# Kernel tuning notes

Measured on AMD Instinct MI355X. Metric: run time of the kernel, lower is better.

Reference implementation:

```python
import jax, jax.numpy as jnp
import numpy as np

B, S, D = 4, 512, 256
NEG = -1e30  # finite stand-in for -inf so fully-masked row 0 stays NaN-free


def setup_inputs() -> dict:
    key = jax.random.key(0)
    ks = jax.random.split(key, 10)
    s = 0.02
    return {
        "x": jax.random.normal(ks[0], (B, S, D), dtype=jnp.float32),
        # edge_mlp: Linear(3D -> D), ReLU, Linear(D -> 1). Stored [in, out].
        "W1": jax.random.normal(ks[1], (3 * D, D), dtype=jnp.float32) * s,
        "b1": jnp.zeros((D,), dtype=jnp.float32),
        "w2": jax.random.normal(ks[2], (D, 1), dtype=jnp.float32) * s,
        "b2": jnp.zeros((1,), dtype=jnp.float32),
        "Wv": jax.random.normal(ks[3], (D, D), dtype=jnp.float32) * s,
        "bv": jnp.zeros((D,), dtype=jnp.float32),
        "Wo": jax.random.normal(ks[4], (D, D), dtype=jnp.float32) * s,
        "bo": jnp.zeros((D,), dtype=jnp.float32),
        "gamma": jnp.ones((D,), dtype=jnp.float32),
        "beta": jnp.zeros((D,), dtype=jnp.float32),
    }


def reference(x, W1, b1, w2, b2, Wv, bv, Wo, bo, gamma, beta):
    b, seq, d = x.shape
    # edge_mlp layer1 on concat([x_i, x_j, x_i - x_j]) decomposes linearly:
    # h[b,i,j,:] = x_i @ (Wa + Wc) + x_j @ (Wb - Wc) + b1
    Wa, Wb, Wc = W1[:d], W1[d:2 * d], W1[2 * d:]
    hi = jnp.einsum('bid,dh->bih', x, Wa + Wc)          # [B,S,D]
    hj = jnp.einsum('bjd,dh->bjh', x, Wb - Wc)          # [B,S,D]
    h = jax.nn.relu(hi[:, :, None, :] + hj[:, None, :, :] + b1)  # [B,S,S,D]
    scores = jnp.einsum('bijh,h->bij', h, w2[:, 0]) + b2[0]      # [B,S,S]
    # strictly-lower-triangular causal mask (j < i)
    mask = jnp.tril(jnp.ones((seq, seq), dtype=bool), k=-1)
    scores = jnp.where(mask, scores, NEG)
    attn = jax.nn.softmax(scores, axis=-1)
    # row i=0 has no valid edges (torch yields NaN there); zero it instead
    row_valid = mask.any(axis=-1)                       # [S]
    attn = attn * row_valid[None, :, None].astype(attn.dtype)
    values = jnp.einsum('bjd,de->bje', x, Wv) + bv      # [B,S,D]
    message = jnp.einsum('bij,bjd->bid', attn, values)  # [B,S,D]
    out = jnp.einsum('bid,de->bie', message, Wo) + bo
    out = x + out
    # LayerNorm over last dim, eps=1e-5, biased variance (torch default)
    mu = jnp.mean(out, axis=-1, keepdims=True)
    var = jnp.mean(jnp.square(out - mu), axis=-1, keepdims=True)
    out = (out - mu) * jax.lax.rsqrt(var + 1e-5) * gamma + beta
    return out
```

## Files before the change

kernel.cpp:

```cpp
#include <hip/hip_runtime.h>
#include <math.h>

#define D 256
#define S 512
#define M 2048

typedef __attribute__((ext_vector_type(8))) short bf16x8;
typedef __attribute__((ext_vector_type(4))) float f32x4;

__device__ inline ushort f2bf(float f) {
    union { float f; unsigned u; } v; v.f = f;
    unsigned r = v.u + 0x7FFFu + ((v.u >> 16) & 1u);
    return (ushort)(r >> 16);
}

__global__ __launch_bounds__(256) void pack_w(
    const float* __restrict__ W1, const float* __restrict__ Wv,
    const float* __restrict__ Wo, ushort* __restrict__ WAt,
    ushort* __restrict__ WBt, ushort* __restrict__ Wvt, ushort* __restrict__ Wot)
{
    const int blk = blockIdx.x, t = threadIdx.x;
    const int mat = blk >> 4;
    const int a0 = ((blk >> 2) & 3) * 64;
    const int b0 = (blk & 3) * 64;
    __shared__ ushort lt[64][72];
    const int r = t >> 4;
    const int c = (t & 15) * 4;
#pragma unroll
    for (int p = 0; p < 4; ++p) {
        const int sr = b0 + p * 16 + r;
        float4 v;
        if (mat == 0) {
            float4 wa = *(const float4*)(W1 + (size_t)sr * 256 + a0 + c);
            float4 wc = *(const float4*)(W1 + (size_t)(512 + sr) * 256 + a0 + c);
            v = make_float4(wa.x + wc.x, wa.y + wc.y, wa.z + wc.z, wa.w + wc.w);
        } else if (mat == 1) {
            float4 wb = *(const float4*)(W1 + (size_t)(256 + sr) * 256 + a0 + c);
            float4 wc = *(const float4*)(W1 + (size_t)(512 + sr) * 256 + a0 + c);
            v = make_float4(wb.x - wc.x, wb.y - wc.y, wb.z - wc.z, wb.w - wc.w);
        } else if (mat == 2) {
            v = *(const float4*)(Wv + (size_t)sr * 256 + a0 + c);
        } else {
            v = *(const float4*)(Wo + (size_t)sr * 256 + a0 + c);
        }
        lt[p * 16 + r][c + 0] = f2bf(v.x);
        lt[p * 16 + r][c + 1] = f2bf(v.y);
        lt[p * 16 + r][c + 2] = f2bf(v.z);
        lt[p * 16 + r][c + 3] = f2bf(v.w);
    }
    __syncthreads();
    ushort* dst = (mat == 0) ? WAt : (mat == 1) ? WBt : (mat == 2) ? Wvt : Wot;
#pragma unroll
    for (int p = 0; p < 4; ++p) {
        const int dr = p * 16 + r;
        ushort4 o = make_ushort4(lt[c + 0][dr], lt[c + 1][dr],
                                 lt[c + 2][dr], lt[c + 3][dr]);
        *(ushort4*)(dst + (size_t)(a0 + dr) * 256 + b0 + c) = o;
    }
}

__global__ __launch_bounds__(256) void gemm_qkv_mfma(
    const float* __restrict__ x, const ushort* __restrict__ WAt,
    const ushort* __restrict__ WBt, const ushort* __restrict__ Wvt,
    const float* __restrict__ b1, const float* __restrict__ bv,
    float* __restrict__ hi, float* __restrict__ hj, ushort* __restrict__ vals_t)
{
    const int bn = blockIdx.x, bm = blockIdx.y;
    const int n0 = bn * 64, m0 = bm * 64;
    const int region = n0 >> 8, c0 = n0 & 255;
    const ushort* Bt = (region == 0) ? WAt : (region == 1) ? WBt : Wvt;
    const int t = threadIdx.x, w = t >> 6, l = t & 63;
    const int q = l >> 4, ln = l & 15;
    const int wm = (w >> 1) * 32, wn = (w & 1) * 32;

    __shared__ ushort T[64][72];

    f32x4 acc[2][2] = {};
    for (int k0 = 0; k0 < 256; k0 += 32) {
        union { bf16x8 v; ushort s[8]; } a[2];
        bf16x8 b[2];
#pragma unroll
        for (int mt = 0; mt < 2; ++mt) {
            const float* xr = x + (size_t)(m0 + wm + mt * 16 + ln) * 256 + k0 + q * 8;
            float4 u0 = *(const float4*)xr;
            float4 u1 = *(const float4*)(xr + 4);
            a[mt].s[0] = f2bf(u0.x); a[mt].s[1] = f2bf(u0.y);
            a[mt].s[2] = f2bf(u0.z); a[mt].s[3] = f2bf(u0.w);
            a[mt].s[4] = f2bf(u1.x); a[mt].s[5] = f2bf(u1.y);
            a[mt].s[6] = f2bf(u1.z); a[mt].s[7] = f2bf(u1.w);
        }
#pragma unroll
        for (int nt = 0; nt < 2; ++nt)
            b[nt] = *(const bf16x8*)(Bt + (size_t)(c0 + wn + nt * 16 + ln) * 256 + k0 + q * 8);
#pragma unroll
        for (int mt = 0; mt < 2; ++mt)
#pragma unroll
            for (int nt = 0; nt < 2; ++nt)
                acc[mt][nt] = __builtin_amdgcn_mfma_f32_16x16x32_bf16(a[mt].v, b[nt], acc[mt][nt], 0, 0, 0);
    }

    if (region < 2) {
        float* dst = (region == 0) ? hi : hj;
#pragma unroll
        for (int nt = 0; nt < 2; ++nt) {
            const int col = c0 + wn + nt * 16 + ln;
            const float bias = (region == 0) ? b1[col] : 0.f;
#pragma unroll
            for (int mt = 0; mt < 2; ++mt)
#pragma unroll
                for (int r = 0; r < 4; ++r) {
                    const int row = m0 + wm + mt * 16 + q * 4 + r;
                    dst[(size_t)row * 256 + col] = acc[mt][nt][r] + bias;
                }
        }
    } else {
#pragma unroll
        for (int nt = 0; nt < 2; ++nt) {
            const int cl = wn + nt * 16 + ln;
            const float bias = bv[c0 + cl];
#pragma unroll
            for (int mt = 0; mt < 2; ++mt)
#pragma unroll
                for (int r = 0; r < 4; ++r)
                    T[cl][wm + mt * 16 + q * 4 + r] = f2bf(acc[mt][nt][r] + bias);
        }
        __syncthreads();
        const int bb = m0 >> 9, jloc = m0 & 511;
#pragma unroll
        for (int p = 0; p < 2; ++p) {
            const int idx = p * 256 + t;
            const int e_l = idx & 63, jc = (idx >> 6) * 8;
            *(uint4*)(vals_t + ((size_t)(bb * 256 + c0 + e_l)) * 512 + jloc + jc) =
                *(const uint4*)&T[e_l][jc];
        }
    }
}

__global__ __launch_bounds__(256) void scores64(
    const float* __restrict__ hi, const float* __restrict__ hj,
    const float* __restrict__ w2, float* __restrict__ sc)
{
    const int jt = blockIdx.x, it = blockIdx.y, bb = blockIdx.z;
    if (jt > 2 * it + 1) return;
    const int i0 = it * 64, j0 = jt * 32;
    const int t = threadIdx.x, w = t >> 6, l = t & 63;
    const int q = l >> 4, ln = l & 15;

    __shared__ __align__(16) float His[32][64];
    __shared__ __align__(16) float Sst[64][36];
    __shared__ float w2s[256];
    if (t < 64) *(float4*)&w2s[t * 4] = *(const float4*)(w2 + t * 4);

    const int si = t & 63, sh = (t >> 6) * 8;
    const float* hisrc = hi + (size_t)((bb << 9) + i0 + si) * 256 + sh;
    const int jrow = w * 8 + q * 2;
    const float* hj0 = hj + (size_t)((bb << 9) + j0 + jrow) * 256;
    const float* hj1 = hj0 + 256;

    float acc00 = 0.f, acc01 = 0.f, acc10 = 0.f, acc11 = 0.f;
    float acc20 = 0.f, acc21 = 0.f, acc30 = 0.f, acc31 = 0.f;

    for (int hc = 0; hc < 256; hc += 32) {
        float4 a0 = *(const float4*)(hisrc + hc);
        float4 a1 = *(const float4*)(hisrc + hc + 4);
        float e0[32], e1[32];
#pragma unroll
        for (int c = 0; c < 8; ++c) {
            *(float4*)&e0[c * 4] = *(const float4*)(hj0 + hc + c * 4);
            *(float4*)&e1[c * 4] = *(const float4*)(hj1 + hc + c * 4);
        }
        __syncthreads();
        His[sh + 0][si] = a0.x; His[sh + 1][si] = a0.y;
        His[sh + 2][si] = a0.z; His[sh + 3][si] = a0.w;
        His[sh + 4][si] = a1.x; His[sh + 5][si] = a1.y;
        His[sh + 6][si] = a1.z; His[sh + 7][si] = a1.w;
        __syncthreads();
#pragma unroll
        for (int h = 0; h < 32; ++h) {
            float4 a = *(const float4*)&His[h][ln * 4];
            const float wv = w2s[hc + h];
            const float f0 = e0[h], f1 = e1[h];
            acc00 += fmaxf(a.x + f0, 0.f) * wv;
            acc01 += fmaxf(a.x + f1, 0.f) * wv;
            acc10 += fmaxf(a.y + f0, 0.f) * wv;
            acc11 += fmaxf(a.y + f1, 0.f) * wv;
            acc20 += fmaxf(a.z + f0, 0.f) * wv;
            acc21 += fmaxf(a.z + f1, 0.f) * wv;
            acc30 += fmaxf(a.w + f0, 0.f) * wv;
            acc31 += fmaxf(a.w + f1, 0.f) * wv;
        }
    }

    Sst[ln * 4 + 0][jrow] = acc00;  Sst[ln * 4 + 0][jrow + 1] = acc01;
    Sst[ln * 4 + 1][jrow] = acc10;  Sst[ln * 4 + 1][jrow + 1] = acc11;
    Sst[ln * 4 + 2][jrow] = acc20;  Sst[ln * 4 + 2][jrow + 1] = acc21;
    Sst[ln * 4 + 3][jrow] = acc30;  Sst[ln * 4 + 3][jrow + 1] = acc31;
    __syncthreads();
    const int i_l = t >> 2, jc = (t & 3) * 8;
    float* dst = sc + ((size_t)bb << 18) + (size_t)(i0 + i_l) * 512 + j0 + jc;
    *(float4*)dst       = *(const float4*)&Sst[i_l][jc];
    *(float4*)(dst + 4) = *(const float4*)&Sst[i_l][jc + 4];
}

__global__ __launch_bounds__(256) void attn_norm(
    const float* __restrict__ sc, ushort* __restrict__ attn_bf)
{
    const int row = blockIdx.x;
    const int b = row >> 9, i = row & 511;
    const int t = threadIdx.x, wave = t >> 6, lane = t & 63;
    ushort* arow = attn_bf + ((size_t)(b << 9) + i) * S;

    if (i == 0) { arow[t] = 0; arow[t + 256] = 0; return; }

    const float* srow = sc + ((size_t)b << 18) + (size_t)i * S;
    __shared__ float s[S];
    __shared__ float red[8];

    float mloc = -3.0e38f;
    for (int j = t; j < i; j += 256) { float v = srow[j]; s[j] = v; mloc = fmaxf(mloc, v); }
#pragma unroll
    for (int off = 32; off; off >>= 1) mloc = fmaxf(mloc, __shfl_xor(mloc, off, 64));
    if (lane == 0) red[wave] = mloc;
    __syncthreads();
    const float mx = fmaxf(fmaxf(red[0], red[1]), fmaxf(red[2], red[3]));

    float sloc = 0.f;
    for (int j = t; j < i; j += 256) {
        float e = __expf(s[j] - mx);
        s[j] = e;
        sloc += e;
    }
#pragma unroll
    for (int off = 32; off; off >>= 1) sloc += __shfl_xor(sloc, off, 64);
    if (lane == 0) red[4 + wave] = sloc;
    __syncthreads();
    const float inv = 1.f / (red[4] + red[5] + red[6] + red[7]);

    for (int j = t; j < S; j += 256)
        arow[j] = (j < i) ? f2bf(s[j] * inv) : (ushort)0;
}

__global__ __launch_bounds__(256) void pv_mfma(
    const ushort* __restrict__ attn_bf, const ushort* __restrict__ vals_t,
    ushort* __restrict__ msg_bf)
{
    const int bn = blockIdx.x, bm = blockIdx.y, b = blockIdx.z;
    const int n0 = bn * 64, m0 = bm * 64;
    const ushort* A = attn_bf + ((size_t)b << 18);
    const ushort* V = vals_t + (size_t)(b * 256) * 512;
    const int t = threadIdx.x, w = t >> 6, l = t & 63;
    const int q = l >> 4, ln = l & 15;
    const int wm = (w >> 1) * 32, wn = (w & 1) * 32;

    f32x4 acc[2][2] = {};
    const int kmax = m0 + 64;
    for (int k0 = 0; k0 < kmax; k0 += 32) {
        bf16x8 a[2], bb[2];
#pragma unroll
        for (int mt = 0; mt < 2; ++mt)
            a[mt] = *(const bf16x8*)(A + (size_t)(m0 + wm + mt * 16 + ln) * S + k0 + q * 8);
#pragma unroll
        for (int nt = 0; nt < 2; ++nt)
            bb[nt] = *(const bf16x8*)(V + (size_t)(n0 + wn + nt * 16 + ln) * 512 + k0 + q * 8);
#pragma unroll
        for (int mt = 0; mt < 2; ++mt)
#pragma unroll
            for (int nt = 0; nt < 2; ++nt)
                acc[mt][nt] = __builtin_amdgcn_mfma_f32_16x16x32_bf16(a[mt], bb[nt], acc[mt][nt], 0, 0, 0);
    }
#pragma unroll
    for (int nt = 0; nt < 2; ++nt) {
        const int col = n0 + wn + nt * 16 + ln;
#pragma unroll
        for (int mt = 0; mt < 2; ++mt)
#pragma unroll
            for (int r = 0; r < 4; ++r) {
                const int row = (b << 9) + m0 + wm + mt * 16 + q * 4 + r;
                msg_bf[(size_t)row * 256 + col] = f2bf(acc[mt][nt][r]);
            }
    }
}

__global__ __launch_bounds__(256) void out_ln_mfma(
    const ushort* __restrict__ msg_bf, const ushort* __restrict__ Wot,
    const float* __restrict__ x, const float* __restrict__ bo,
    const float* __restrict__ gamma, const float* __restrict__ beta,
    float* __restrict__ out)
{
    const int r0 = blockIdx.x * 16;
    const int t = threadIdx.x, w = t >> 6, l = t & 63;
    const int q = l >> 4, ln = l & 15;

    __shared__ float redS[16][4], redQ[16][4];

    f32x4 acc[4] = {};
    for (int k0 = 0; k0 < 256; k0 += 32) {
        bf16x8 a = *(const bf16x8*)(msg_bf + (size_t)(r0 + ln) * 256 + k0 + q * 8);
#pragma unroll
        for (int nt = 0; nt < 4; ++nt) {
            bf16x8 bb = *(const bf16x8*)(Wot + (size_t)(w * 64 + nt * 16 + ln) * 256 + k0 + q * 8);
            acc[nt] = __builtin_amdgcn_mfma_f32_16x16x32_bf16(a, bb, acc[nt], 0, 0, 0);
        }
    }

    float sum[4] = {}, sq[4] = {};
#pragma unroll
    for (int nt = 0; nt < 4; ++nt) {
        const int col = w * 64 + nt * 16 + ln;
        const float bov = bo[col];
#pragma unroll
        for (int r = 0; r < 4; ++r) {
            const int row = r0 + q * 4 + r;
            float v = acc[nt][r] + x[(size_t)row * 256 + col] + bov;
            acc[nt][r] = v;
            sum[r] += v;
            sq[r] += v * v;
        }
    }
#pragma unroll
    for (int r = 0; r < 4; ++r) {
#pragma unroll
        for (int off = 1; off < 16; off <<= 1) {
            sum[r] += __shfl_xor(sum[r], off, 64);
            sq[r]  += __shfl_xor(sq[r],  off, 64);
        }
    }
    if (ln == 0) {
#pragma unroll
        for (int r = 0; r < 4; ++r) {
            redS[q * 4 + r][w] = sum[r];
            redQ[q * 4 + r][w] = sq[r];
        }
    }
    __syncthreads();
#pragma unroll
    for (int nt = 0; nt < 4; ++nt) {
        const int col = w * 64 + nt * 16 + ln;
        const float g = gamma[col], be = beta[col];
#pragma unroll
        for (int r = 0; r < 4; ++r) {
            const int rl = q * 4 + r;
            const float ts = redS[rl][0] + redS[rl][1] + redS[rl][2] + redS[rl][3];
            const float tq = redQ[rl][0] + redQ[rl][1] + redQ[rl][2] + redQ[rl][3];
            const float mu = ts * (1.f / 256.f);
            const float var = tq * (1.f / 256.f) - mu * mu;
            out[(size_t)(r0 + rl) * 256 + col] =
                (acc[nt][r] - mu) * rsqrtf(var + 1e-5f) * g + be;
        }
    }
}

extern "C" void kernel_launch(void* const* d_in, const int* in_sizes, int n_in,
                              void* d_out, int out_size, void* d_ws, size_t ws_size,
                              hipStream_t stream)
{
    (void)in_sizes; (void)n_in; (void)out_size; (void)ws_size;
    const float* x     = (const float*)d_in[0];
    const float* W1    = (const float*)d_in[1];
    const float* b1    = (const float*)d_in[2];
    const float* w2    = (const float*)d_in[3];
    const float* Wv    = (const float*)d_in[5];
    const float* bv    = (const float*)d_in[6];
    const float* Wo    = (const float*)d_in[7];
    const float* bo    = (const float*)d_in[8];
    const float* gamma = (const float*)d_in[9];
    const float* beta  = (const float*)d_in[10];
    float* out = (float*)d_out;

    float* ws = (float*)d_ws;
    const size_t CH = 64 * 1024;
    float*  hi      = ws;
    float*  hj      = ws + 8 * CH;
    float*  sc      = ws + 16 * CH;
    ushort* WAt     = (ushort*)(ws + 32 * CH);
    ushort* WBt     = (ushort*)(ws + 33 * CH);
    ushort* Wvt     = (ushort*)(ws + 34 * CH);
    ushort* Wot     = (ushort*)(ws + 35 * CH);
    ushort* vals_t  = (ushort*)(ws + 36 * CH);
    ushort* attn_bf = (ushort*)(ws + 40 * CH);
    ushort* msg_bf  = (ushort*)(ws + 48 * CH);

    pack_w       <<<dim3(64),        256, 0, stream>>>(W1, Wv, Wo, WAt, WBt, Wvt, Wot);
    gemm_qkv_mfma<<<dim3(12, 32),    256, 0, stream>>>(x, WAt, WBt, Wvt, b1, bv, hi, hj, vals_t);
    scores64     <<<dim3(16, 8, 4),  256, 0, stream>>>(hi, hj, w2, sc);
    attn_norm    <<<dim3(M),         256, 0, stream>>>(sc, attn_bf);
    pv_mfma      <<<dim3(4, 8, 4),   256, 0, stream>>>(attn_bf, vals_t, msg_bf);
    out_ln_mfma  <<<dim3(128),       256, 0, stream>>>(msg_bf, Wot, x, bo, gamma, beta, out);
}
```

Before: 141.0 us.

## Fuse softmax, PV matmul and output projection with LayerNorm into one kernel

Replaces the three kernels attn_norm, pv_mfma and out_ln_mfma with a single attn_out kernel. Each block handles 16 query rows of one batch: it computes the softmax into shared memory as bf16, does the causal PV MFMA up to the row bound, stages the message in shared memory, then runs the Wo projection, residual add and LayerNorm. This removes two launches and the global round trips of the attention and message buffers. In exchange there are only 128 blocks and the softmax reads each score row three times per wave, so there is less parallelism and more redundant exp work.

```diff
diff --git a/kernel.cpp b/kernel.cpp
--- a/kernel.cpp
+++ b/kernel.cpp
@@ -202,104 +202,69 @@
     *(float4*)(dst + 4) = *(const float4*)&Sst[i_l][jc + 4];
 }
 
-__global__ __launch_bounds__(256) void attn_norm(
-    const float* __restrict__ sc, ushort* __restrict__ attn_bf)
-{
-    const int row = blockIdx.x;
-    const int b = row >> 9, i = row & 511;
-    const int t = threadIdx.x, wave = t >> 6, lane = t & 63;
-    ushort* arow = attn_bf + ((size_t)(b << 9) + i) * S;
-
-    if (i == 0) { arow[t] = 0; arow[t + 256] = 0; return; }
-
-    const float* srow = sc + ((size_t)b << 18) + (size_t)i * S;
-    __shared__ float s[S];
-    __shared__ float red[8];
-
-    float mloc = -3.0e38f;
-    for (int j = t; j < i; j += 256) { float v = srow[j]; s[j] = v; mloc = fmaxf(mloc, v); }
-#pragma unroll
-    for (int off = 32; off; off >>= 1) mloc = fmaxf(mloc, __shfl_xor(mloc, off, 64));
-    if (lane == 0) red[wave] = mloc;
-    __syncthreads();
-    const float mx = fmaxf(fmaxf(red[0], red[1]), fmaxf(red[2], red[3]));
-
-    float sloc = 0.f;
-    for (int j = t; j < i; j += 256) {
-        float e = __expf(s[j] - mx);
-        s[j] = e;
-        sloc += e;
-    }
-#pragma unroll
-    for (int off = 32; off; off >>= 1) sloc += __shfl_xor(sloc, off, 64);
-    if (lane == 0) red[4 + wave] = sloc;
-    __syncthreads();
-    const float inv = 1.f / (red[4] + red[5] + red[6] + red[7]);
-
-    for (int j = t; j < S; j += 256)
-        arow[j] = (j < i) ? f2bf(s[j] * inv) : (ushort)0;
-}
-
-__global__ __launch_bounds__(256) void pv_mfma(
-    const ushort* __restrict__ attn_bf, const ushort* __restrict__ vals_t,
-    ushort* __restrict__ msg_bf)
-{
-    const int bn = blockIdx.x, bm = blockIdx.y, b = blockIdx.z;
-    const int n0 = bn * 64, m0 = bm * 64;
-    const ushort* A = attn_bf + ((size_t)b << 18);
-    const ushort* V = vals_t + (size_t)(b * 256) * 512;
+__global__ __launch_bounds__(256) void attn_out(
+    const float* __restrict__ sc, const ushort* __restrict__ vals_t,
+    const ushort* __restrict__ Wot, const float* __restrict__ x,
+    const float* __restrict__ bo, const float* __restrict__ gamma,
+    const float* __restrict__ beta, float* __restrict__ out)
+{
+    const int it = blockIdx.x, b = blockIdx.y;
+    const int i0 = it * 16;
+    const int KTp = (i0 + 16 + 31) & ~31;
     const int t = threadIdx.x, w = t >> 6, l = t & 63;
     const int q = l >> 4, ln = l & 15;
-    const int wm = (w >> 1) * 32, wn = (w & 1) * 32;
-
-    f32x4 acc[2][2] = {};
-    const int kmax = m0 + 64;
-    for (int k0 = 0; k0 < kmax; k0 += 32) {
-        bf16x8 a[2], bb[2];
-#pragma unroll
-        for (int mt = 0; mt < 2; ++mt)
-            a[mt] = *(const bf16x8*)(A + (size_t)(m0 + wm + mt * 16 + ln) * S + k0 + q * 8);
-#pragma unroll
-        for (int nt = 0; nt < 2; ++nt)
-            bb[nt] = *(const bf16x8*)(V + (size_t)(n0 + wn + nt * 16 + ln) * 512 + k0 + q * 8);
-#pragma unroll
-        for (int mt = 0; mt < 2; ++mt)
-#pragma unroll
-            for (int nt = 0; nt < 2; ++nt)
-                acc[mt][nt] = __builtin_amdgcn_mfma_f32_16x16x32_bf16(a[mt], bb[nt], acc[mt][nt], 0, 0, 0);
-    }
-#pragma unroll
-    for (int nt = 0; nt < 2; ++nt) {
-        const int col = n0 + wn + nt * 16 + ln;
-#pragma unroll
-        for (int mt = 0; mt < 2; ++mt)
-#pragma unroll
-            for (int r = 0; r < 4; ++r) {
-                const int row = (b << 9) + m0 + wm + mt * 16 + q * 4 + r;
-                msg_bf[(size_t)row * 256 + col] = f2bf(acc[mt][nt][r]);
-            }
-    }
-}
-
-__global__ __launch_bounds__(256) void out_ln_mfma(
-    const ushort* __restrict__ msg_bf, const ushort* __restrict__ Wot,
-    const float* __restrict__ x, const float* __restrict__ bo,
-    const float* __restrict__ gamma, const float* __restrict__ beta,
-    float* __restrict__ out)
-{
-    const int r0 = blockIdx.x * 16;
-    const int t = threadIdx.x, w = t >> 6, l = t & 63;
-    const int q = l >> 4, ln = l & 15;
-
+
+    __shared__ ushort P[16][520];
+    __shared__ ushort Msg[16][264];
     __shared__ float redS[16][4], redQ[16][4];
 
+    const float* scb = sc + ((size_t)b << 18);
+
+    for (int rr = 0; rr < 4; ++rr) {
+        const int r = w * 4 + rr;
+        const int i = i0 + r;
+        for (int j = l; j < KTp; j += 64) P[r][j] = 0;
+        if (i > 0) {
+            const float* srow = scb + (size_t)i * S;
+            float m = -3.0e38f;
+            for (int j = l; j < i; j += 64) m = fmaxf(m, srow[j]);
+#pragma unroll
+            for (int off = 32; off; off >>= 1) m = fmaxf(m, __shfl_xor(m, off, 64));
+            float s = 0.f;
+            for (int j = l; j < i; j += 64) s += __expf(srow[j] - m);
+#pragma unroll
+            for (int off = 32; off; off >>= 1) s += __shfl_xor(s, off, 64);
+            const float inv = 1.f / s;
+            for (int j = l; j < i; j += 64)
+                P[r][j] = f2bf(__expf(srow[j] - m) * inv);
+        }
+    }
+    __syncthreads();
+
+    const ushort* V = vals_t + (size_t)(b * 256) * 512;
     f32x4 acc[4] = {};
+    for (int k0 = 0; k0 < KTp; k0 += 32) {
+        bf16x8 a = *(const bf16x8*)&P[ln][k0 + q * 8];
+#pragma unroll
+        for (int nt = 0; nt < 4; ++nt) {
+            bf16x8 bb = *(const bf16x8*)(V + (size_t)(w * 64 + nt * 16 + ln) * 512 + k0 + q * 8);
+            acc[nt] = __builtin_amdgcn_mfma_f32_16x16x32_bf16(a, bb, acc[nt], 0, 0, 0);
+        }
+    }
+#pragma unroll
+    for (int nt = 0; nt < 4; ++nt)
+#pragma unroll
+        for (int r = 0; r < 4; ++r)
+            Msg[q * 4 + r][w * 64 + nt * 16 + ln] = f2bf(acc[nt][r]);
+    __syncthreads();
+
+    f32x4 acc2[4] = {};
     for (int k0 = 0; k0 < 256; k0 += 32) {
-        bf16x8 a = *(const bf16x8*)(msg_bf + (size_t)(r0 + ln) * 256 + k0 + q * 8);
+        bf16x8 a = *(const bf16x8*)&Msg[ln][k0 + q * 8];
 #pragma unroll
         for (int nt = 0; nt < 4; ++nt) {
             bf16x8 bb = *(const bf16x8*)(Wot + (size_t)(w * 64 + nt * 16 + ln) * 256 + k0 + q * 8);
-            acc[nt] = __builtin_amdgcn_mfma_f32_16x16x32_bf16(a, bb, acc[nt], 0, 0, 0);
+            acc2[nt] = __builtin_amdgcn_mfma_f32_16x16x32_bf16(a, bb, acc2[nt], 0, 0, 0);
         }
     }
 
@@ -310,9 +275,9 @@
         const float bov = bo[col];
 #pragma unroll
         for (int r = 0; r < 4; ++r) {
-            const int row = r0 + q * 4 + r;
-            float v = acc[nt][r] + x[(size_t)row * 256 + col] + bov;
-            acc[nt][r] = v;
+            const int grow = (b << 9) + i0 + q * 4 + r;
+            float v = acc2[nt][r] + x[(size_t)grow * 256 + col] + bov;
+            acc2[nt][r] = v;
             sum[r] += v;
             sq[r] += v * v;
         }
@@ -344,8 +309,9 @@
             const float tq = redQ[rl][0] + redQ[rl][1] + redQ[rl][2] + redQ[rl][3];
             const float mu = ts * (1.f / 256.f);
             const float var = tq * (1.f / 256.f) - mu * mu;
-            out[(size_t)(r0 + rl) * 256 + col] =
-                (acc[nt][r] - mu) * rsqrtf(var + 1e-5f) * g + be;
+            const int grow = (b << 9) + i0 + rl;
+            out[(size_t)grow * 256 + col] =
+                (acc2[nt][r] - mu) * rsqrtf(var + 1e-5f) * g + be;
         }
     }
 }
@@ -377,13 +343,9 @@
     ushort* Wvt     = (ushort*)(ws + 34 * CH);
     ushort* Wot     = (ushort*)(ws + 35 * CH);
     ushort* vals_t  = (ushort*)(ws + 36 * CH);
-    ushort* attn_bf = (ushort*)(ws + 40 * CH);
-    ushort* msg_bf  = (ushort*)(ws + 48 * CH);
 
     pack_w       <<<dim3(64),        256, 0, stream>>>(W1, Wv, Wo, WAt, WBt, Wvt, Wot);
     gemm_qkv_mfma<<<dim3(12, 32),    256, 0, stream>>>(x, WAt, WBt, Wvt, b1, bv, hi, hj, vals_t);
     scores64     <<<dim3(16, 8, 4),  256, 0, stream>>>(hi, hj, w2, sc);
-    attn_norm    <<<dim3(M),         256, 0, stream>>>(sc, attn_bf);
-    pv_mfma      <<<dim3(4, 8, 4),   256, 0, stream>>>(attn_bf, vals_t, msg_bf);
-    out_ln_mfma  <<<dim3(128),       256, 0, stream>>>(msg_bf, Wot, x, bo, gamma, beta, out);
-}
+    attn_out     <<<dim3(32, 4),     256, 0, stream>>>(sc, vals_t, Wot, x, bo, gamma, beta, out);
+}
```

Result: slower. 148.3 us (+5.1%).

## Fuse softmax into PV MFMA kernel with deferred normalization in LDS

Applied to the files above, without the earlier changes.

Removes the separate attn_norm kernel and the bf16 attention matrix round-trip through global memory. Each PV block now computes the row max and unnormalized exponentials for its 64 rows directly from the fp32 scores into shared memory, then applies the 1/sum scaling at the output store. This saves one launch and a global write/read of the attention matrix. In exchange, the softmax is recomputed redundantly by the 4 column blocks, and the single-wave-per-row serial softmax loop adds latency before the MFMA loop starts.

```diff
diff --git a/kernel.cpp b/kernel.cpp
--- a/kernel.cpp
+++ b/kernel.cpp
@@ -202,63 +202,50 @@
     *(float4*)(dst + 4) = *(const float4*)&Sst[i_l][jc + 4];
 }
 
-__global__ __launch_bounds__(256) void attn_norm(
-    const float* __restrict__ sc, ushort* __restrict__ attn_bf)
-{
-    const int row = blockIdx.x;
-    const int b = row >> 9, i = row & 511;
-    const int t = threadIdx.x, wave = t >> 6, lane = t & 63;
-    ushort* arow = attn_bf + ((size_t)(b << 9) + i) * S;
-
-    if (i == 0) { arow[t] = 0; arow[t + 256] = 0; return; }
-
-    const float* srow = sc + ((size_t)b << 18) + (size_t)i * S;
-    __shared__ float s[S];
-    __shared__ float red[8];
-
-    float mloc = -3.0e38f;
-    for (int j = t; j < i; j += 256) { float v = srow[j]; s[j] = v; mloc = fmaxf(mloc, v); }
-#pragma unroll
-    for (int off = 32; off; off >>= 1) mloc = fmaxf(mloc, __shfl_xor(mloc, off, 64));
-    if (lane == 0) red[wave] = mloc;
-    __syncthreads();
-    const float mx = fmaxf(fmaxf(red[0], red[1]), fmaxf(red[2], red[3]));
-
-    float sloc = 0.f;
-    for (int j = t; j < i; j += 256) {
-        float e = __expf(s[j] - mx);
-        s[j] = e;
-        sloc += e;
-    }
-#pragma unroll
-    for (int off = 32; off; off >>= 1) sloc += __shfl_xor(sloc, off, 64);
-    if (lane == 0) red[4 + wave] = sloc;
-    __syncthreads();
-    const float inv = 1.f / (red[4] + red[5] + red[6] + red[7]);
-
-    for (int j = t; j < S; j += 256)
-        arow[j] = (j < i) ? f2bf(s[j] * inv) : (ushort)0;
-}
-
-__global__ __launch_bounds__(256) void pv_mfma(
-    const ushort* __restrict__ attn_bf, const ushort* __restrict__ vals_t,
+__global__ __launch_bounds__(256) void pv_sm(
+    const float* __restrict__ sc, const ushort* __restrict__ vals_t,
     ushort* __restrict__ msg_bf)
 {
     const int bn = blockIdx.x, bm = blockIdx.y, b = blockIdx.z;
     const int n0 = bn * 64, m0 = bm * 64;
-    const ushort* A = attn_bf + ((size_t)b << 18);
-    const ushort* V = vals_t + (size_t)(b * 256) * 512;
+    const int kmax = m0 + 64;
     const int t = threadIdx.x, w = t >> 6, l = t & 63;
     const int q = l >> 4, ln = l & 15;
     const int wm = (w >> 1) * 32, wn = (w & 1) * 32;
 
+    __shared__ ushort P[64][520];
+    __shared__ float invS[64];
+
+    const float* scb = sc + ((size_t)b << 18);
+    for (int rr = 0; rr < 16; ++rr) {
+        const int r = w * 16 + rr;
+        const int i = m0 + r;
+        for (int j = l; j < kmax; j += 64) P[r][j] = 0;
+        if (i == 0) { if (l == 0) invS[r] = 0.f; continue; }
+        const float* srow = scb + (size_t)i * S;
+        float mx = -3.0e38f;
+        for (int j = l; j < i; j += 64) mx = fmaxf(mx, srow[j]);
+#pragma unroll
+        for (int off = 32; off; off >>= 1) mx = fmaxf(mx, __shfl_xor(mx, off, 64));
+        float s = 0.f;
+        for (int j = l; j < i; j += 64) {
+            float e = __expf(srow[j] - mx);
+            P[r][j] = f2bf(e);
+            s += e;
+        }
+#pragma unroll
+        for (int off = 32; off; off >>= 1) s += __shfl_xor(s, off, 64);
+        if (l == 0) invS[r] = 1.f / s;
+    }
+    __syncthreads();
+
+    const ushort* V = vals_t + (size_t)(b * 256) * 512;
     f32x4 acc[2][2] = {};
-    const int kmax = m0 + 64;
     for (int k0 = 0; k0 < kmax; k0 += 32) {
         bf16x8 a[2], bb[2];
 #pragma unroll
         for (int mt = 0; mt < 2; ++mt)
-            a[mt] = *(const bf16x8*)(A + (size_t)(m0 + wm + mt * 16 + ln) * S + k0 + q * 8);
+            a[mt] = *(const bf16x8*)&P[wm + mt * 16 + ln][k0 + q * 8];
 #pragma unroll
         for (int nt = 0; nt < 2; ++nt)
             bb[nt] = *(const bf16x8*)(V + (size_t)(n0 + wn + nt * 16 + ln) * 512 + k0 + q * 8);
@@ -275,8 +262,9 @@
         for (int mt = 0; mt < 2; ++mt)
 #pragma unroll
             for (int r = 0; r < 4; ++r) {
-                const int row = (b << 9) + m0 + wm + mt * 16 + q * 4 + r;
-                msg_bf[(size_t)row * 256 + col] = f2bf(acc[mt][nt][r]);
+                const int rl = wm + mt * 16 + q * 4 + r;
+                const int row = (b << 9) + m0 + rl;
+                msg_bf[(size_t)row * 256 + col] = f2bf(acc[mt][nt][r] * invS[rl]);
             }
     }
 }
@@ -377,13 +365,11 @@
     ushort* Wvt     = (ushort*)(ws + 34 * CH);
     ushort* Wot     = (ushort*)(ws + 35 * CH);
     ushort* vals_t  = (ushort*)(ws + 36 * CH);
-    ushort* attn_bf = (ushort*)(ws + 40 * CH);
-    ushort* msg_bf  = (ushort*)(ws + 48 * CH);
+    ushort* msg_bf  = (ushort*)(ws + 40 * CH);
 
     pack_w       <<<dim3(64),        256, 0, stream>>>(W1, Wv, Wo, WAt, WBt, Wvt, Wot);
     gemm_qkv_mfma<<<dim3(12, 32),    256, 0, stream>>>(x, WAt, WBt, Wvt, b1, bv, hi, hj, vals_t);
     scores64     <<<dim3(16, 8, 4),  256, 0, stream>>>(hi, hj, w2, sc);
-    attn_norm    <<<dim3(M),         256, 0, stream>>>(sc, attn_bf);
-    pv_mfma      <<<dim3(4, 8, 4),   256, 0, stream>>>(attn_bf, vals_t, msg_bf);
+    pv_sm        <<<dim3(4, 8, 4),   256, 0, stream>>>(sc, vals_t, msg_bf);
     out_ln_mfma  <<<dim3(128),       256, 0, stream>>>(msg_bf, Wot, x, bo, gamma, beta, out);
 }
```

New measurement: 182.4 us. 1.29x slower.
